# Kernel optimization log

Hardware: AMD Instinct MI355X
Metric: run time of the kernel (lower is better)

## Reference

```python
import jax, jax.numpy as jnp
import numpy as np
from math import sqrt

D_LLM = 768
N_HEADS = 8
D_KEYS = 128


def setup_inputs() -> dict:
    key = jax.random.key(0)
    ks = jax.random.split(key, 9)
    B, T, N, S = 8, 96, 16, 1000
    dkh = D_KEYS * N_HEADS
    inp = {
        "time_series": jax.random.normal(ks[0], (B, T, N), dtype=jnp.float32),
        "source_embedding": jax.random.normal(ks[1], (S, D_LLM), dtype=jnp.float32),
        "value_embedding": jax.random.normal(ks[2], (S, D_LLM), dtype=jnp.float32),
        # key_projection: Linear(d_llm, d_keys*n_heads)
        "Wk": jax.random.normal(ks[3], (D_LLM, dkh), dtype=jnp.float32) / np.float32(sqrt(D_LLM)),
        "bk": jnp.zeros((dkh,), dtype=jnp.float32),
        # value_projection: Linear(d_llm, d_keys*n_heads)
        "Wv": jax.random.normal(ks[4], (D_LLM, dkh), dtype=jnp.float32) / np.float32(sqrt(D_LLM)),
        "bv": jnp.zeros((dkh,), dtype=jnp.float32),
        # out_projection: Linear(d_keys*n_heads, d_llm)
        "Wo": jax.random.normal(ks[5], (dkh, D_LLM), dtype=jnp.float32) / np.float32(sqrt(dkh)),
        "bo": jnp.zeros((D_LLM,), dtype=jnp.float32),
    }
    return inp


def reference(time_series, source_embedding, value_embedding, Wk, bk, Wv, bv, Wo, bo):
    B, T, N = time_series.shape
    S = source_embedding.shape[0]
    H, dk = N_HEADS, D_KEYS

    # (B,T,N) -> (B*N, T); Q repeats each scalar across d_keys*n_heads then nan->0
    ts = jnp.transpose(time_series, (0, 2, 1)).reshape(B * N, T)
    ts = jnp.where(jnp.isnan(ts), jnp.float32(0.0), ts)
    Q = jnp.broadcast_to(ts[:, :, None, None], (B * N, T, H, dk))  # bthe

    K = (source_embedding @ Wk + bk).reshape(S, H, dk)  # she
    V = (value_embedding @ Wv + bv).reshape(S, H, dk)   # she

    scale = jnp.float32(1.0 / sqrt(dk))
    scores = jnp.einsum('bthe,she->bhts', Q, K)          # [B*N, H, T, S]
    A = jax.nn.softmax(scale * scores, axis=-1)          # dropout = identity (eval)
    out = jnp.einsum('bhts,she->bthe', A, V).reshape(B * N, T, H * dk)
    return out @ Wo + bo                                 # [B*N, T, d_llm]
```

## Files before the change

kernel.cpp:

```cpp
#include <hip/hip_runtime.h>
#include <hip/hip_bf16.h>
#include <math.h>

#define D_LLM 768
#define DKH   1024
#define NH    8
#define DK    128
#define S_LEN 1000
#define S_PAD 1024
#define M_ROWS 12288
#define T_LEN 96
#define N_VARS 16

static constexpr float SCALE_EXP2 = (float)(0.08838834764831845 * 1.4426950408889634);

typedef __attribute__((ext_vector_type(8))) _Float16 half8;
typedef __attribute__((ext_vector_type(2))) _Float16 half2v;
typedef __attribute__((ext_vector_type(4))) float f32x4;

__device__ __forceinline__ half2v pkrtz(float a, float b) {
    return __builtin_bit_cast(half2v, __builtin_amdgcn_cvt_pkrtz(a, b));
}

__device__ __forceinline__ void gload_lds16(const void* g, void* l) {
    __builtin_amdgcn_global_load_lds(
        (const __attribute__((address_space(1))) unsigned int*)g,
        (__attribute__((address_space(3))) unsigned int*)l, 16, 0, 0);
}

__global__ __launch_bounds__(256) void prep_kernel(const float* __restrict__ vemb,
                                                   const float* __restrict__ Wv,
                                                   const float* __restrict__ Wo,
                                                   const float* __restrict__ Wk,
                                                   const float* __restrict__ bk,
                                                   _Float16* __restrict__ Ab16,
                                                   _Float16* __restrict__ Wvt,
                                                   _Float16* __restrict__ Wot,
                                                   float* __restrict__ Wksum,
                                                   float* __restrict__ bksum) {
    __shared__ float tl[32][33];
    int blk = blockIdx.x, tid = threadIdx.x;
    if (blk < 768) {
        int i4 = (blk * 256 + tid) * 4;
        float4 v = make_float4(0.f, 0.f, 0.f, 0.f);
        if (i4 < S_LEN * D_LLM) v = *(const float4*)(vemb + i4);
        short4 o;
        o.x = __builtin_bit_cast(short, (_Float16)v.x);
        o.y = __builtin_bit_cast(short, (_Float16)v.y);
        o.z = __builtin_bit_cast(short, (_Float16)v.z);
        o.w = __builtin_bit_cast(short, (_Float16)v.w);
        *(short4*)(Ab16 + i4) = o;
    } else if (blk < 1536) {
        int tau = blk - 768;
        int k0 = (tau % 24) * 32, n0 = (tau / 24) * 32;
        int tx = tid & 31, ty = tid >> 5;
        #pragma unroll
        for (int p = 0; p < 4; ++p)
            tl[ty + p * 8][tx] = Wv[(size_t)(k0 + ty + p * 8) * DKH + n0 + tx];
        __syncthreads();
        #pragma unroll
        for (int p = 0; p < 4; ++p)
            Wvt[(size_t)(n0 + ty + p * 8) * D_LLM + k0 + tx] = (_Float16)tl[tx][ty + p * 8];
    } else if (blk < 2304) {
        int tau = blk - 1536;
        int k0 = (tau & 31) * 32, n0 = (tau >> 5) * 32;
        int tx = tid & 31, ty = tid >> 5;
        #pragma unroll
        for (int p = 0; p < 4; ++p)
            tl[ty + p * 8][tx] = Wo[(size_t)(k0 + ty + p * 8) * D_LLM + n0 + tx];
        __syncthreads();
        #pragma unroll
        for (int p = 0; p < 4; ++p)
            Wot[(size_t)(n0 + ty + p * 8) * DKH + k0 + tx] = (_Float16)tl[tx][ty + p * 8];
    } else {
        int blk2 = blk - 2304;
        int w = tid >> 6, lane = tid & 63;
        if (blk2 < 192) {
            int d = blk2 * 4 + w;
            const float* p = Wk + (size_t)d * DKH + lane * 16;
            float s = 0.f;
            #pragma unroll
            for (int i = 0; i < 4; ++i) {
                float4 v = *(const float4*)(p + i * 4);
                s += v.x + v.y + v.z + v.w;
            }
            s += __shfl_down(s, 4);
            s += __shfl_down(s, 2);
            s += __shfl_down(s, 1);
            if ((lane & 7) == 0) Wksum[d * NH + (lane >> 3)] = s;
        } else if (w == 0) {
            const float* p = bk + lane * 16;
            float s = 0.f;
            #pragma unroll
            for (int i = 0; i < 4; ++i) {
                float4 v = *(const float4*)(p + i * 4);
                s += v.x + v.y + v.z + v.w;
            }
            s += __shfl_down(s, 4);
            s += __shfl_down(s, 2);
            s += __shfl_down(s, 1);
            if ((lane & 7) == 0) bksum[lane >> 3] = s;
        }
    }
}

__global__ __launch_bounds__(256) void kv_kernel(const float* __restrict__ src,
                                                 const float* __restrict__ Wksum,
                                                 const float* __restrict__ bksum,
                                                 float* __restrict__ Kpad,
                                                 const _Float16* __restrict__ A,
                                                 const _Float16* __restrict__ Bt,
                                                 const float* __restrict__ bias,
                                                 _Float16* __restrict__ Vt) {
    __shared__ _Float16 VAs[2][2048];
    __shared__ _Float16 VBs[2][2048];
    int tid = threadIdx.x;
    if (blockIdx.x < 256) {
        int w = tid >> 6, lane = tid & 63;
        int s = blockIdx.x * 4 + w;
        if (s >= S_LEN) {
            if (lane < 8) Kpad[lane * S_PAD + s] = 0.f;
            return;
        }
        const float* sp = src + (size_t)s * D_LLM + lane * 12;
        float xv[12];
        ((float4*)xv)[0] = *(const float4*)(sp);
        ((float4*)xv)[1] = *(const float4*)(sp + 4);
        ((float4*)xv)[2] = *(const float4*)(sp + 8);
        float a[8] = {0.f, 0.f, 0.f, 0.f, 0.f, 0.f, 0.f, 0.f};
        const float* wp = Wksum + lane * 12 * NH;
        #pragma unroll
        for (int i = 0; i < 12; ++i) {
            float4 wa = *(const float4*)(wp + i * 8);
            float4 wb = *(const float4*)(wp + i * 8 + 4);
            a[0] = fmaf(xv[i], wa.x, a[0]); a[1] = fmaf(xv[i], wa.y, a[1]);
            a[2] = fmaf(xv[i], wa.z, a[2]); a[3] = fmaf(xv[i], wa.w, a[3]);
            a[4] = fmaf(xv[i], wb.x, a[4]); a[5] = fmaf(xv[i], wb.y, a[5]);
            a[6] = fmaf(xv[i], wb.z, a[6]); a[7] = fmaf(xv[i], wb.w, a[7]);
        }
        #pragma unroll
        for (int off = 32; off > 0; off >>= 1) {
            #pragma unroll
            for (int hh = 0; hh < 8; ++hh) a[hh] += __shfl_xor(a[hh], off);
        }
        #pragma unroll
        for (int hh = 0; hh < 8; ++hh)
            if (lane == hh) Kpad[hh * S_PAD + s] = (a[hh] + bksum[hh]) * SCALE_EXP2;
        return;
    }
    int b2 = blockIdx.x - 256;
    int w = tid >> 6, lane = tid & 63;
    int bm0 = (b2 >> 4) * 64, bn0 = (b2 & 15) * 64;
    int lrow = tid >> 2, lcol = (tid & 3) * 8;
    const _Float16* ga = A + (size_t)(bm0 + lrow) * D_LLM + lcol;
    const _Float16* gb = Bt + (size_t)(bn0 + lrow) * D_LLM + lcol;

    f32x4 acc[2][2];
    #pragma unroll
    for (int m = 0; m < 2; ++m)
        #pragma unroll
        for (int n = 0; n < 2; ++n) acc[m][n] = (f32x4){0.f, 0.f, 0.f, 0.f};
    int sgrp = (lane >> 4) << 3;
    int arow = (w >> 1) * 32 + (lane & 15);
    int brow = (w & 1) * 32 + (lane & 15);

#define VSTAGE(buf, k0) do { \
        gload_lds16(ga + (k0), (char*)&VAs[buf][0] + w * 1024); \
        gload_lds16(gb + (k0), (char*)&VBs[buf][0] + w * 1024); } while (0)

    VSTAGE(0, 0);
    __syncthreads();
    #pragma unroll 2
    for (int tt = 0; tt < 24; ++tt) {
        int cur = tt & 1;
        if (tt < 23) VSTAGE(cur ^ 1, (tt + 1) * 32);
        const _Float16* Ac = &VAs[cur][0];
        const _Float16* Bc = &VBs[cur][0];
        half8 af[2], bf[2];
        #pragma unroll
        for (int m = 0; m < 2; ++m) af[m] = *(const half8*)(Ac + (arow + m * 16) * 32 + sgrp);
        #pragma unroll
        for (int n = 0; n < 2; ++n) bf[n] = *(const half8*)(Bc + (brow + n * 16) * 32 + sgrp);
        __builtin_amdgcn_s_setprio(1);
        #pragma unroll
        for (int m = 0; m < 2; ++m)
            #pragma unroll
            for (int n = 0; n < 2; ++n)
                acc[m][n] = __builtin_amdgcn_mfma_f32_16x16x32_f16(af[m], bf[n], acc[m][n], 0, 0, 0);
        __builtin_amdgcn_s_setprio(0);
        __syncthreads();
    }
#undef VSTAGE

    int rowoff = (lane >> 4) << 2;
    #pragma unroll
    for (int m = 0; m < 2; ++m) {
        #pragma unroll
        for (int n = 0; n < 2; ++n) {
            int c = bn0 + (w & 1) * 32 + n * 16 + (lane & 15);
            float b = bias[c];
            #pragma unroll
            for (int q = 0; q < 4; ++q) {
                int srow = bm0 + (w >> 1) * 32 + m * 16 + rowoff + q;
                float val = (srow < S_LEN) ? acc[m][n][q] + b : 0.f;
                Vt[(size_t)c * S_PAD + srow] = (_Float16)val;
            }
        }
    }
}

__device__ __forceinline__ void compute_afr(const float* kq, float x0, float x1,
                                            float nm0, float nm1, half8& o0, half8& o1) {
    float4 a = *(const float4*)kq;
    float4 b = *(const float4*)(kq + 4);
    float kv[8] = {a.x, a.y, a.z, a.w, b.x, b.y, b.z, b.w};
    union { half8 v; half2v h[4]; } u0, u1;
    #pragma unroll
    for (int j = 0; j < 4; ++j) {
        float w00 = __builtin_amdgcn_exp2f(fmaf(x0, kv[2 * j], nm0));
        float w01 = __builtin_amdgcn_exp2f(fmaf(x0, kv[2 * j + 1], nm0));
        u0.h[j] = pkrtz(w00, w01);
        float w10 = __builtin_amdgcn_exp2f(fmaf(x1, kv[2 * j], nm1));
        float w11 = __builtin_amdgcn_exp2f(fmaf(x1, kv[2 * j + 1], nm1));
        u1.h[j] = pkrtz(w10, w11);
    }
    o0 = u0.v; o1 = u1.v;
}

__global__ __launch_bounds__(256) void attn_mfma_kernel(const float* __restrict__ ts,
                                                        const float* __restrict__ Kpad,
                                                        const _Float16* __restrict__ Vt,
                                                        _Float16* __restrict__ attB) {
    __shared__ _Float16 Vs[3][8192];
    __shared__ float Krow[1024];
    __shared__ float red[8];
    const int tid = threadIdx.x;
    const int lane = tid & 63, w = tid >> 6;
    const int h = blockIdx.y;
    const int m0 = (blockIdx.x * 4 + w) * 32;
    const int l15 = lane & 15, q = lane >> 4;

    const int erow = w * 8 + (lane >> 3);
    const int sgl = ((lane & 7) ^ (lane >> 3)) * 8;
    const _Float16* gsrc = Vt + (size_t)(h * DK + erow) * S_PAD + sgl;
    const float* kg = Kpad + h * S_PAD;

    gload_lds16(kg + w * 256 + lane * 4, (char*)Krow + w * 1024);
    #pragma unroll
    for (int i = 0; i < 4; ++i)
        gload_lds16(gsrc + (size_t)(i * 32) * S_PAD, (char*)&Vs[0][0] + i * 4096 + w * 1024);
    #pragma unroll
    for (int i = 0; i < 4; ++i)
        gload_lds16(gsrc + (size_t)(i * 32) * S_PAD + 64, (char*)&Vs[1][0] + i * 4096 + w * 1024);

    float x0, x1;
    {
        int m = m0 + l15;
        int rr = m / T_LEN;
        float v = ts[((size_t)(rr >> 4) * T_LEN + (m % T_LEN)) * N_VARS + (rr & 15)];
        x0 = (v != v) ? 0.f : v;
        m = m0 + 16 + l15;
        rr = m / T_LEN;
        v = ts[((size_t)(rr >> 4) * T_LEN + (m % T_LEN)) * N_VARS + (rr & 15)];
        x1 = (v != v) ? 0.f : v;
    }

    asm volatile("s_waitcnt vmcnt(8)" ::: "memory");
    __builtin_amdgcn_sched_barrier(0);
    __builtin_amdgcn_s_barrier();

    float mn, mx;
    {
        float4 k4 = *(const float4*)&Krow[tid * 4];
        if (tid < 250) {
            mx = fmaxf(fmaxf(k4.x, k4.y), fmaxf(k4.z, k4.w));
            mn = fminf(fminf(k4.x, k4.y), fminf(k4.z, k4.w));
        } else { mx = -3e38f; mn = 3e38f; }
        #pragma unroll
        for (int off = 32; off > 0; off >>= 1) {
            mx = fmaxf(mx, __shfl_xor(mx, off));
            mn = fminf(mn, __shfl_xor(mn, off));
        }
        if (lane == 0) { red[w * 2] = mn; red[w * 2 + 1] = mx; }
        asm volatile("s_waitcnt lgkmcnt(0)" ::: "memory");
        __builtin_amdgcn_sched_barrier(0);
        __builtin_amdgcn_s_barrier();
        mn = fminf(fminf(red[0], red[2]), fminf(red[4], red[6]));
        mx = fmaxf(fmaxf(red[1], red[3]), fmaxf(red[5], red[7]));
    }

    float nm0 = -((x0 >= 0.f) ? x0 * mx : x0 * mn);
    float nm1 = -((x1 >= 0.f) ? x1 * mx : x1 * mn);
    float wpadf0, wpadf1;
    {
        half2v p0 = pkrtz(__builtin_amdgcn_exp2f(nm0), 0.f);
        half2v p1 = pkrtz(__builtin_amdgcn_exp2f(nm1), 0.f);
        wpadf0 = (float)p0[0];
        wpadf1 = (float)p1[0];
    }

    f32x4 acc0[8], acc1[8];
    #pragma unroll
    for (int e = 0; e < 8; ++e) {
        acc0[e] = (f32x4){0.f, 0.f, 0.f, 0.f};
        acc1[e] = (f32x4){0.f, 0.f, 0.f, 0.f};
    }
    f32x4 accd0 = (f32x4){0.f, 0.f, 0.f, 0.f};
    f32x4 accd1 = (f32x4){0.f, 0.f, 0.f, 0.f};
    half8 ones;
    #pragma unroll
    for (int j = 0; j < 8; ++j) ones[j] = (_Float16)1.0f;

    const float* kvp = Krow + q * 8;
    half8 afrA0, afrA1, afrB0, afrB1;
    compute_afr(kvp, x0, x1, nm0, nm1, afrA0, afrA1);

    const int bofs0 = l15 * 128 + ((q * 16) ^ ((l15 & 7) << 4));
    const int bofs1 = l15 * 128 + ((64 + q * 16) ^ ((l15 & 7) << 4));

#define PVSTEP(AF0, AF1, BOFS) do { \
        __builtin_amdgcn_s_setprio(1); \
        _Pragma("unroll") \
        for (int e = 0; e < 8; ++e) { \
            half8 bfv = *(const half8*)(cb + e * 2048 + (BOFS)); \
            acc0[e] = __builtin_amdgcn_mfma_f32_16x16x32_f16(AF0, bfv, acc0[e], 0, 0, 0); \
            acc1[e] = __builtin_amdgcn_mfma_f32_16x16x32_f16(AF1, bfv, acc1[e], 0, 0, 0); \
        } \
        accd0 = __builtin_amdgcn_mfma_f32_16x16x32_f16(AF0, ones, accd0, 0, 0, 0); \
        accd1 = __builtin_amdgcn_mfma_f32_16x16x32_f16(AF1, ones, accd1, 0, 0, 0); \
        __builtin_amdgcn_s_setprio(0); } while (0)

    #pragma unroll
    for (int kt = 0; kt < 16; ++kt) {
        if (kt == 15) asm volatile("s_waitcnt vmcnt(0)" ::: "memory");
        else         asm volatile("s_waitcnt vmcnt(4)" ::: "memory");
        __builtin_amdgcn_sched_barrier(0);
        __builtin_amdgcn_s_barrier();
        if (kt < 14) {
            char* d = (char*)&Vs[0][0] + ((kt + 2) % 3) * 16384 + w * 1024;
            #pragma unroll
            for (int i = 0; i < 4; ++i)
                gload_lds16(gsrc + (size_t)(i * 32) * S_PAD + (kt + 2) * 64, d + i * 4096);
        }
        const char* cb = (const char*)&Vs[0][0] + (kt % 3) * 16384;
        compute_afr(kvp + kt * 64 + 32, x0, x1, nm0, nm1, afrB0, afrB1);
        PVSTEP(afrA0, afrA1, bofs0);
        if (kt < 15) compute_afr(kvp + (kt + 1) * 64, x0, x1, nm0, nm1, afrA0, afrA1);
        PVSTEP(afrB0, afrB1, bofs1);
    }
#undef PVSTEP

    int rowoff = q << 2;
    #pragma unroll
    for (int r = 0; r < 2; ++r) {
        #pragma unroll
        for (int qq = 0; qq < 4; ++qq) {
            float wp = __shfl(r ? wpadf1 : wpadf0, rowoff + qq);
            float den = (r ? accd1[qq] : accd0[qq]) - 24.f * wp;
            float inv = 1.f / den;
            int mrow = m0 + r * 16 + rowoff + qq;
            _Float16* op = attB + (size_t)mrow * DKH + h * DK + l15;
            #pragma unroll
            for (int e = 0; e < 8; ++e)
                op[e * 16] = (_Float16)((r ? acc1[e][qq] : acc0[e][qq]) * inv);
        }
    }
}

__global__ __launch_bounds__(256) void outproj_kernel(const _Float16* __restrict__ A,
                                                      const _Float16* __restrict__ Bt,
                                                      const float* __restrict__ bo,
                                                      float* __restrict__ C) {
    __shared__ _Float16 As[3][4096];
    __shared__ _Float16 Bs[3][3072];
    int wg = blockIdx.x;
    wg = (wg & 7) * 96 + (wg >> 3);
    int bx = wg & 7, by = wg >> 3;
    int t = threadIdx.x, w = t >> 6, lane = t & 63;
    int bm0 = by * 128, bn0 = bx * 96;
    int lrow = t >> 2, lcol = (t & 3) * 8;
    const _Float16* ga0 = A + (size_t)(bm0 + lrow) * DKH + lcol;
    const _Float16* ga1 = ga0 + (size_t)64 * DKH;
    const _Float16* gb0 = Bt + (size_t)(bn0 + lrow) * DKH + lcol;
    const _Float16* gb1 = gb0 + (size_t)64 * DKH;

    f32x4 acc[4][3];
    #pragma unroll
    for (int m = 0; m < 4; ++m)
        #pragma unroll
        for (int n = 0; n < 3; ++n) acc[m][n] = (f32x4){0.f, 0.f, 0.f, 0.f};

    int sgrp = (lane >> 4) << 3;
    int arow = (w >> 1) * 64 + (lane & 15);
    int brow = (w & 1) * 48 + (lane & 15);

#define OSTAGE(bi, k0) do { \
        gload_lds16(ga0 + (k0), (char*)&As[bi][0] + w * 1024); \
        gload_lds16(ga1 + (k0), (char*)&As[bi][0] + 4096 + w * 1024); \
        gload_lds16(gb0 + (k0), (char*)&Bs[bi][0] + w * 1024); \
        if (w < 2) gload_lds16(gb1 + (k0), (char*)&Bs[bi][0] + 4096 + w * 1024); } while (0)

    OSTAGE(0, 0);
    OSTAGE(1, 32);
    #pragma unroll
    for (int kt = 0; kt < 32; ++kt) {
        if (kt == 31)   asm volatile("s_waitcnt vmcnt(0)" ::: "memory");
        else if (w < 2) asm volatile("s_waitcnt vmcnt(4)" ::: "memory");
        else            asm volatile("s_waitcnt vmcnt(3)" ::: "memory");
        __builtin_amdgcn_sched_barrier(0);
        __builtin_amdgcn_s_barrier();
        if (kt < 30) OSTAGE((kt + 2) % 3, (kt + 2) * 32);
        const _Float16* Ac = &As[kt % 3][0];
        const _Float16* Bc = &Bs[kt % 3][0];
        half8 af[4], bf[3];
        #pragma unroll
        for (int m = 0; m < 4; ++m) af[m] = *(const half8*)(Ac + (arow + m * 16) * 32 + sgrp);
        #pragma unroll
        for (int n = 0; n < 3; ++n) bf[n] = *(const half8*)(Bc + (brow + n * 16) * 32 + sgrp);
        __builtin_amdgcn_s_setprio(1);
        #pragma unroll
        for (int m = 0; m < 4; ++m)
            #pragma unroll
            for (int n = 0; n < 3; ++n)
                acc[m][n] = __builtin_amdgcn_mfma_f32_16x16x32_f16(af[m], bf[n], acc[m][n], 0, 0, 0);
        __builtin_amdgcn_s_setprio(0);
    }
#undef OSTAGE

    int rowoff = (lane >> 4) << 2;
    #pragma unroll
    for (int m = 0; m < 4; ++m) {
        #pragma unroll
        for (int n = 0; n < 3; ++n) {
            int col = bn0 + (w & 1) * 48 + n * 16 + (lane & 15);
            float b = bo[col];
            #pragma unroll
            for (int q = 0; q < 4; ++q) {
                int row = bm0 + (w >> 1) * 64 + m * 16 + rowoff + q;
                C[(size_t)row * D_LLM + col] = acc[m][n][q] + b;
            }
        }
    }
}

extern "C" void kernel_launch(void* const* d_in, const int* in_sizes, int n_in,
                              void* d_out, int out_size, void* d_ws, size_t ws_size,
                              hipStream_t stream) {
    const float* ts   = (const float*)d_in[0];
    const float* src  = (const float*)d_in[1];
    const float* vemb = (const float*)d_in[2];
    const float* Wk   = (const float*)d_in[3];
    const float* bk   = (const float*)d_in[4];
    const float* Wv   = (const float*)d_in[5];
    const float* bv   = (const float*)d_in[6];
    const float* Wo   = (const float*)d_in[7];
    const float* bo   = (const float*)d_in[8];
    float* out = (float*)d_out;

    float* ws = (float*)d_ws;
    float* Kpad   = ws;
    float* Wksum  = ws + 8192;
    float* bksum  = ws + 14336;
    _Float16* Vt   = (_Float16*)(ws + 14592);
    _Float16* Wot  = (_Float16*)(ws + 540672);
    _Float16* attB = (_Float16*)(ws + 936960);
    _Float16* Ab16 = (_Float16*)(ws + 936960);
    _Float16* Wvt  = (_Float16*)(ws + 1330176);

    prep_kernel<<<2497, 256, 0, stream>>>(vemb, Wv, Wo, Wk, bk, Ab16, Wvt, Wot, Wksum, bksum);
    kv_kernel<<<512, 256, 0, stream>>>(src, Wksum, bksum, Kpad, Ab16, Wvt, bv, Vt);
    {
        dim3 g(96, NH);
        attn_mfma_kernel<<<g, 256, 0, stream>>>(ts, Kpad, Vt, attB);
    }
    outproj_kernel<<<768, 256, 0, stream>>>(attB, Wot, bo, out);
}
```

Before: 87.95 us.

## Split attention head dim across two blocks with finer 4-stage V pipeline

The attention kernel grid gains a third dimension that splits each head's 128 value columns into two halves, so twice as many blocks run and each holds half the accumulators. The V tile pipeline now loads 32-key chunks into a 4-buffer ring instead of 64-key chunks in a 3-buffer ring, which shrinks LDS use and changes the swizzle. The cost is that the softmax weights (exp2) and denominator MFMAs are computed twice, once per half, and there are more barriers per key.

```diff
diff --git a/kernel.cpp b/kernel.cpp
--- a/kernel.cpp
+++ b/kernel.cpp
@@ -231,27 +231,25 @@
                                                         const float* __restrict__ Kpad,
                                                         const _Float16* __restrict__ Vt,
                                                         _Float16* __restrict__ attB) {
-    __shared__ _Float16 Vs[3][8192];
+    __shared__ _Float16 Vs[4][2048];
     __shared__ float Krow[1024];
     __shared__ float red[8];
     const int tid = threadIdx.x;
     const int lane = tid & 63, w = tid >> 6;
     const int h = blockIdx.y;
-    const int m0 = (blockIdx.x * 4 + w) * 32;
+    const int eh = blockIdx.z;
+    const int m0 = blockIdx.x * 128 + w * 32;
     const int l15 = lane & 15, q = lane >> 4;
 
-    const int erow = w * 8 + (lane >> 3);
-    const int sgl = ((lane & 7) ^ (lane >> 3)) * 8;
-    const _Float16* gsrc = Vt + (size_t)(h * DK + erow) * S_PAD + sgl;
+    const int erow = w * 16 + (lane >> 2);
+    const int perm = (lane & 3) ^ (erow & 3);
+    const _Float16* gsrc = Vt + (size_t)(h * DK + eh * 64 + erow) * S_PAD + perm * 8;
     const float* kg = Kpad + h * S_PAD;
 
     gload_lds16(kg + w * 256 + lane * 4, (char*)Krow + w * 1024);
-    #pragma unroll
-    for (int i = 0; i < 4; ++i)
-        gload_lds16(gsrc + (size_t)(i * 32) * S_PAD, (char*)&Vs[0][0] + i * 4096 + w * 1024);
-    #pragma unroll
-    for (int i = 0; i < 4; ++i)
-        gload_lds16(gsrc + (size_t)(i * 32) * S_PAD + 64, (char*)&Vs[1][0] + i * 4096 + w * 1024);
+    gload_lds16(gsrc, (char*)&Vs[0][0] + w * 1024);
+    gload_lds16(gsrc + 32, (char*)&Vs[1][0] + w * 1024);
+    gload_lds16(gsrc + 64, (char*)&Vs[2][0] + w * 1024);
 
     float x0, x1;
     {
@@ -265,7 +263,7 @@
         x1 = (v != v) ? 0.f : v;
     }
 
-    asm volatile("s_waitcnt vmcnt(8)" ::: "memory");
+    asm volatile("s_waitcnt vmcnt(3)" ::: "memory");
     __builtin_amdgcn_sched_barrier(0);
     __builtin_amdgcn_s_barrier();
 
@@ -299,9 +297,9 @@
         wpadf1 = (float)p1[0];
     }
 
-    f32x4 acc0[8], acc1[8];
-    #pragma unroll
-    for (int e = 0; e < 8; ++e) {
+    f32x4 acc0[4], acc1[4];
+    #pragma unroll
+    for (int e = 0; e < 4; ++e) {
         acc0[e] = (f32x4){0.f, 0.f, 0.f, 0.f};
         acc1[e] = (f32x4){0.f, 0.f, 0.f, 0.f};
     }
@@ -315,40 +313,29 @@
     half8 afrA0, afrA1, afrB0, afrB1;
     compute_afr(kvp, x0, x1, nm0, nm1, afrA0, afrA1);
 
-    const int bofs0 = l15 * 128 + ((q * 16) ^ ((l15 & 7) << 4));
-    const int bofs1 = l15 * 128 + ((64 + q * 16) ^ ((l15 & 7) << 4));
-
-#define PVSTEP(AF0, AF1, BOFS) do { \
-        __builtin_amdgcn_s_setprio(1); \
-        _Pragma("unroll") \
-        for (int e = 0; e < 8; ++e) { \
-            half8 bfv = *(const half8*)(cb + e * 2048 + (BOFS)); \
-            acc0[e] = __builtin_amdgcn_mfma_f32_16x16x32_f16(AF0, bfv, acc0[e], 0, 0, 0); \
-            acc1[e] = __builtin_amdgcn_mfma_f32_16x16x32_f16(AF1, bfv, acc1[e], 0, 0, 0); \
-        } \
-        accd0 = __builtin_amdgcn_mfma_f32_16x16x32_f16(AF0, ones, accd0, 0, 0, 0); \
-        accd1 = __builtin_amdgcn_mfma_f32_16x16x32_f16(AF1, ones, accd1, 0, 0, 0); \
-        __builtin_amdgcn_s_setprio(0); } while (0)
-
-    #pragma unroll
-    for (int kt = 0; kt < 16; ++kt) {
-        if (kt == 15) asm volatile("s_waitcnt vmcnt(0)" ::: "memory");
-        else         asm volatile("s_waitcnt vmcnt(4)" ::: "memory");
+    const int vofs = l15 * 64 + (((q ^ (l15 & 3)) & 3) << 4);
+
+    #pragma unroll
+    for (int kt = 0; kt < 32; ++kt) {
+        if (kt < 30)      asm volatile("s_waitcnt vmcnt(2)" ::: "memory");
+        else if (kt == 30) asm volatile("s_waitcnt vmcnt(1)" ::: "memory");
+        else               asm volatile("s_waitcnt vmcnt(0)" ::: "memory");
         __builtin_amdgcn_sched_barrier(0);
         __builtin_amdgcn_s_barrier();
-        if (kt < 14) {
-            char* d = (char*)&Vs[0][0] + ((kt + 2) % 3) * 16384 + w * 1024;
-            #pragma unroll
-            for (int i = 0; i < 4; ++i)
-                gload_lds16(gsrc + (size_t)(i * 32) * S_PAD + (kt + 2) * 64, d + i * 4096);
-        }
-        const char* cb = (const char*)&Vs[0][0] + (kt % 3) * 16384;
-        compute_afr(kvp + kt * 64 + 32, x0, x1, nm0, nm1, afrB0, afrB1);
-        PVSTEP(afrA0, afrA1, bofs0);
-        if (kt < 15) compute_afr(kvp + (kt + 1) * 64, x0, x1, nm0, nm1, afrA0, afrA1);
-        PVSTEP(afrB0, afrB1, bofs1);
-    }
-#undef PVSTEP
+        if (kt <= 28)
+            gload_lds16(gsrc + (kt + 3) * 32, (char*)&Vs[(kt + 3) & 3][0] + w * 1024);
+        const char* cb = (const char*)&Vs[kt & 3][0];
+        if (kt < 31) compute_afr(kvp + (kt + 1) * 32, x0, x1, nm0, nm1, afrB0, afrB1);
+        #pragma unroll
+        for (int et = 0; et < 4; ++et) {
+            half8 bfv = *(const half8*)(cb + et * 1024 + vofs);
+            acc0[et] = __builtin_amdgcn_mfma_f32_16x16x32_f16(afrA0, bfv, acc0[et], 0, 0, 0);
+            acc1[et] = __builtin_amdgcn_mfma_f32_16x16x32_f16(afrA1, bfv, acc1[et], 0, 0, 0);
+        }
+        accd0 = __builtin_amdgcn_mfma_f32_16x16x32_f16(afrA0, ones, accd0, 0, 0, 0);
+        accd1 = __builtin_amdgcn_mfma_f32_16x16x32_f16(afrA1, ones, accd1, 0, 0, 0);
+        afrA0 = afrB0; afrA1 = afrB1;
+    }
 
     int rowoff = q << 2;
     #pragma unroll
@@ -359,10 +346,10 @@
             float den = (r ? accd1[qq] : accd0[qq]) - 24.f * wp;
             float inv = 1.f / den;
             int mrow = m0 + r * 16 + rowoff + qq;
-            _Float16* op = attB + (size_t)mrow * DKH + h * DK + l15;
-            #pragma unroll
-            for (int e = 0; e < 8; ++e)
-                op[e * 16] = (_Float16)((r ? acc1[e][qq] : acc0[e][qq]) * inv);
+            _Float16* op = attB + (size_t)mrow * DKH + h * DK + eh * 64 + l15;
+            #pragma unroll
+            for (int et = 0; et < 4; ++et)
+                op[et * 16] = (_Float16)((r ? acc1[et][qq] : acc0[et][qq]) * inv);
         }
     }
 }
@@ -470,7 +457,7 @@
     prep_kernel<<<2497, 256, 0, stream>>>(vemb, Wv, Wo, Wk, bk, Ab16, Wvt, Wot, Wksum, bksum);
     kv_kernel<<<512, 256, 0, stream>>>(src, Wksum, bksum, Kpad, Ab16, Wvt, bv, Vt);
     {
-        dim3 g(96, NH);
+        dim3 g(96, NH, 2);
         attn_mfma_kernel<<<g, 256, 0, stream>>>(ts, Kpad, Vt, attB);
     }
     outproj_kernel<<<768, 256, 0, stream>>>(attB, Wot, bo, out);
```

Measured after the change: 98.79 us. 12.3% more time.

## Precompute per-head K min/max in separate kernel and double-buffer V in attention

Applied to the files above, without the earlier changes.

Adds a tiny kernel that computes each head's key min/max once, so attention blocks no longer stage K into LDS and run a block-wide reduction. K values are now read directly from global memory (through cache) inside compute_afr. The V pipeline goes from triple to double buffering with two barriers per step, and the loop is only partly unrolled. This lowers LDS use and prologue latency, at the cost of an extra launch, global K reads inside the loop and less load/compute overlap.

```diff
diff --git a/kernel.cpp b/kernel.cpp
--- a/kernel.cpp
+++ b/kernel.cpp
@@ -209,6 +209,22 @@
     }
 }
 
+__global__ __launch_bounds__(64) void kminmax_kernel(const float* __restrict__ Kpad,
+                                                     float* __restrict__ mnmx) {
+    int h = blockIdx.x, lane = threadIdx.x;
+    float mx = -1e30f, mn = 1e30f;
+    for (int s = lane; s < S_LEN; s += 64) {
+        float v = Kpad[h * S_PAD + s];
+        mx = fmaxf(mx, v); mn = fminf(mn, v);
+    }
+    #pragma unroll
+    for (int off = 32; off > 0; off >>= 1) {
+        mx = fmaxf(mx, __shfl_xor(mx, off));
+        mn = fminf(mn, __shfl_xor(mn, off));
+    }
+    if (lane == 0) { mnmx[h * 2] = mn; mnmx[h * 2 + 1] = mx; }
+}
+
 __device__ __forceinline__ void compute_afr(const float* kq, float x0, float x1,
                                             float nm0, float nm1, half8& o0, half8& o1) {
     float4 a = *(const float4*)kq;
@@ -229,11 +245,10 @@
 
 __global__ __launch_bounds__(256) void attn_mfma_kernel(const float* __restrict__ ts,
                                                         const float* __restrict__ Kpad,
+                                                        const float* __restrict__ mnmx,
                                                         const _Float16* __restrict__ Vt,
                                                         _Float16* __restrict__ attB) {
-    __shared__ _Float16 Vs[3][8192];
-    __shared__ float Krow[1024];
-    __shared__ float red[8];
+    __shared__ _Float16 Vs[2][8192];
     const int tid = threadIdx.x;
     const int lane = tid & 63, w = tid >> 6;
     const int h = blockIdx.y;
@@ -243,54 +258,21 @@
     const int erow = w * 8 + (lane >> 3);
     const int sgl = ((lane & 7) ^ (lane >> 3)) * 8;
     const _Float16* gsrc = Vt + (size_t)(h * DK + erow) * S_PAD + sgl;
-    const float* kg = Kpad + h * S_PAD;
-
-    gload_lds16(kg + w * 256 + lane * 4, (char*)Krow + w * 1024);
-    #pragma unroll
-    for (int i = 0; i < 4; ++i)
-        gload_lds16(gsrc + (size_t)(i * 32) * S_PAD, (char*)&Vs[0][0] + i * 4096 + w * 1024);
-    #pragma unroll
-    for (int i = 0; i < 4; ++i)
-        gload_lds16(gsrc + (size_t)(i * 32) * S_PAD + 64, (char*)&Vs[1][0] + i * 4096 + w * 1024);
-
-    float x0, x1;
+
+    float mn = mnmx[h * 2], mx = mnmx[h * 2 + 1];
+    float x0, x1, nm0, nm1;
     {
         int m = m0 + l15;
         int rr = m / T_LEN;
         float v = ts[((size_t)(rr >> 4) * T_LEN + (m % T_LEN)) * N_VARS + (rr & 15)];
         x0 = (v != v) ? 0.f : v;
+        nm0 = -((x0 >= 0.f) ? x0 * mx : x0 * mn);
         m = m0 + 16 + l15;
         rr = m / T_LEN;
         v = ts[((size_t)(rr >> 4) * T_LEN + (m % T_LEN)) * N_VARS + (rr & 15)];
         x1 = (v != v) ? 0.f : v;
-    }
-
-    asm volatile("s_waitcnt vmcnt(8)" ::: "memory");
-    __builtin_amdgcn_sched_barrier(0);
-    __builtin_amdgcn_s_barrier();
-
-    float mn, mx;
-    {
-        float4 k4 = *(const float4*)&Krow[tid * 4];
-        if (tid < 250) {
-            mx = fmaxf(fmaxf(k4.x, k4.y), fmaxf(k4.z, k4.w));
-            mn = fminf(fminf(k4.x, k4.y), fminf(k4.z, k4.w));
-        } else { mx = -3e38f; mn = 3e38f; }
-        #pragma unroll
-        for (int off = 32; off > 0; off >>= 1) {
-            mx = fmaxf(mx, __shfl_xor(mx, off));
-            mn = fminf(mn, __shfl_xor(mn, off));
-        }
-        if (lane == 0) { red[w * 2] = mn; red[w * 2 + 1] = mx; }
-        asm volatile("s_waitcnt lgkmcnt(0)" ::: "memory");
-        __builtin_amdgcn_sched_barrier(0);
-        __builtin_amdgcn_s_barrier();
-        mn = fminf(fminf(red[0], red[2]), fminf(red[4], red[6]));
-        mx = fmaxf(fmaxf(red[1], red[3]), fmaxf(red[5], red[7]));
-    }
-
-    float nm0 = -((x0 >= 0.f) ? x0 * mx : x0 * mn);
-    float nm1 = -((x1 >= 0.f) ? x1 * mx : x1 * mn);
+        nm1 = -((x1 >= 0.f) ? x1 * mx : x1 * mn);
+    }
     float wpadf0, wpadf1;
     {
         half2v p0 = pkrtz(__builtin_amdgcn_exp2f(nm0), 0.f);
@@ -311,9 +293,18 @@
     #pragma unroll
     for (int j = 0; j < 8; ++j) ones[j] = (_Float16)1.0f;
 
-    const float* kvp = Krow + q * 8;
+    const float* kvp = Kpad + h * S_PAD + q * 8;
     half8 afrA0, afrA1, afrB0, afrB1;
     compute_afr(kvp, x0, x1, nm0, nm1, afrA0, afrA1);
+
+    #pragma unroll
+    for (int i = 0; i < 4; ++i)
+        gload_lds16(gsrc + (size_t)(i * 32) * S_PAD, (char*)&Vs[0][0] + i * 4096 + w * 1024);
+    #pragma unroll
+    for (int i = 0; i < 4; ++i)
+        gload_lds16(gsrc + (size_t)(i * 32) * S_PAD + 64, (char*)&Vs[1][0] + i * 4096 + w * 1024);
+    asm volatile("s_waitcnt vmcnt(4)" ::: "memory");
+    __builtin_amdgcn_s_barrier();
 
     const int bofs0 = l15 * 128 + ((q * 16) ^ ((l15 & 7) << 4));
     const int bofs1 = l15 * 128 + ((64 + q * 16) ^ ((l15 & 7) << 4));
@@ -330,23 +321,24 @@
         accd1 = __builtin_amdgcn_mfma_f32_16x16x32_f16(AF1, ones, accd1, 0, 0, 0); \
         __builtin_amdgcn_s_setprio(0); } while (0)
 
-    #pragma unroll
+    #pragma unroll 2
     for (int kt = 0; kt < 16; ++kt) {
-        if (kt == 15) asm volatile("s_waitcnt vmcnt(0)" ::: "memory");
-        else         asm volatile("s_waitcnt vmcnt(4)" ::: "memory");
-        __builtin_amdgcn_sched_barrier(0);
-        __builtin_amdgcn_s_barrier();
-        if (kt < 14) {
-            char* d = (char*)&Vs[0][0] + ((kt + 2) % 3) * 16384 + w * 1024;
-            #pragma unroll
-            for (int i = 0; i < 4; ++i)
-                gload_lds16(gsrc + (size_t)(i * 32) * S_PAD + (kt + 2) * 64, d + i * 4096);
-        }
-        const char* cb = (const char*)&Vs[0][0] + (kt % 3) * 16384;
+        const char* cb = (const char*)&Vs[0][0] + (kt & 1) * 16384;
         compute_afr(kvp + kt * 64 + 32, x0, x1, nm0, nm1, afrB0, afrB1);
         PVSTEP(afrA0, afrA1, bofs0);
         if (kt < 15) compute_afr(kvp + (kt + 1) * 64, x0, x1, nm0, nm1, afrA0, afrA1);
         PVSTEP(afrB0, afrB1, bofs1);
+        __builtin_amdgcn_s_barrier();
+        if (kt < 14) {
+            #pragma unroll
+            for (int i = 0; i < 4; ++i)
+                gload_lds16(gsrc + (size_t)(i * 32) * S_PAD + (kt + 2) * 64,
+                            (char*)&Vs[0][0] + (kt & 1) * 16384 + i * 4096 + w * 1024);
+            asm volatile("s_waitcnt vmcnt(4)" ::: "memory");
+        } else {
+            asm volatile("s_waitcnt vmcnt(0)" ::: "memory");
+        }
+        __builtin_amdgcn_s_barrier();
     }
 #undef PVSTEP
 
@@ -461,6 +453,7 @@
     float* Kpad   = ws;
     float* Wksum  = ws + 8192;
     float* bksum  = ws + 14336;
+    float* mnmx   = ws + 14352;
     _Float16* Vt   = (_Float16*)(ws + 14592);
     _Float16* Wot  = (_Float16*)(ws + 540672);
     _Float16* attB = (_Float16*)(ws + 936960);
@@ -469,9 +462,10 @@
 
     prep_kernel<<<2497, 256, 0, stream>>>(vemb, Wv, Wo, Wk, bk, Ab16, Wvt, Wot, Wksum, bksum);
     kv_kernel<<<512, 256, 0, stream>>>(src, Wksum, bksum, Kpad, Ab16, Wvt, bv, Vt);
+    kminmax_kernel<<<8, 64, 0, stream>>>(Kpad, mnmx);
     {
         dim3 g(96, NH);
-        attn_mfma_kernel<<<g, 256, 0, stream>>>(ts, Kpad, Vt, attB);
+        attn_mfma_kernel<<<g, 256, 0, stream>>>(ts, Kpad, mnmx, Vt, attB);
     }
     outproj_kernel<<<768, 256, 0, stream>>>(attB, Wot, bo, out);
 }
```

New measurement: 98.17 us. 1.12x slower.
